# Kernel tuning notes

Hardware: AMD Instinct MI355X
Metric: run time of the kernel (lower is better)

The kernel has to match this reference:

```python
import jax, jax.numpy as jnp
import numpy as np

DIM = 1536
N_HEADS = 12
HEAD_DIM = DIM // N_HEADS  # 128
EPS = 1e-6
B, L = 2, 2048


def _rms_norm(x, g, eps=EPS):
    # WanRMSNorm: normalize in fp32 over last dim, scale by g
    xf = x.astype(jnp.float32)
    y = xf * jax.lax.rsqrt(jnp.mean(xf * xf, axis=-1, keepdims=True) + eps)
    return (y * g).astype(x.dtype)


def _apply_rotary(x, freqs):
    # x: [b, s, n, d]; freqs: [1, s, 2d] -> cos/sin each [1, s, 1, d]
    cos, sin = jnp.split(freqs[:, :, None, :], 2, axis=-1)
    b, s, n, d = x.shape
    xr = x.reshape(b, s, n, d // 2, 2)
    rot = jnp.stack([-xr[..., 1], xr[..., 0]], axis=-1).reshape(b, s, n, d)
    out = x.astype(jnp.float32) * cos + rot.astype(jnp.float32) * sin
    return out.astype(x.dtype)


def setup_inputs() -> dict:
    key = jax.random.key(0)
    ks = jax.random.split(key, 12)
    scale = 1.0 / np.sqrt(DIM)
    x = jax.random.normal(ks[0], (B, L, DIM), dtype=jnp.float32)
    wq = jax.random.normal(ks[1], (DIM, DIM), dtype=jnp.float32) * scale
    bq = jnp.zeros((DIM,), dtype=jnp.float32)
    wk = jax.random.normal(ks[2], (DIM, DIM), dtype=jnp.float32) * scale
    bk = jnp.zeros((DIM,), dtype=jnp.float32)
    wv = jax.random.normal(ks[3], (DIM, DIM), dtype=jnp.float32) * scale
    bv = jnp.zeros((DIM,), dtype=jnp.float32)
    wo = jax.random.normal(ks[4], (DIM, DIM), dtype=jnp.float32) * scale
    bo = jnp.zeros((DIM,), dtype=jnp.float32)
    gq = jnp.ones((DIM,), dtype=jnp.float32)
    gk = jnp.ones((DIM,), dtype=jnp.float32)
    # real RoPE table: interleaved-pair cos/sin, concatenated -> [1, L, 2*HEAD_DIM]
    half = HEAD_DIM // 2
    inv_freq = 1.0 / (10000.0 ** (np.arange(half, dtype=np.float32) / half))
    ang = np.arange(L, dtype=np.float32)[:, None] * inv_freq[None, :]  # [L, half]
    cos = np.repeat(np.cos(ang), 2, axis=-1)  # [L, HEAD_DIM]
    sin = np.repeat(np.sin(ang), 2, axis=-1)
    freqs = jnp.asarray(np.concatenate([cos, sin], axis=-1)[None])  # [1, L, 2*HEAD_DIM]
    seq_lens = jnp.array([L, 3 * L // 4], dtype=jnp.int32)
    grid_sizes = jnp.array([[16, 16, 8], [16, 12, 8]], dtype=jnp.int32)
    return {"x": x, "wq": wq, "bq": bq, "wk": wk, "bk": bk, "wv": wv, "bv": bv,
            "wo": wo, "bo": bo, "gq": gq, "gk": gk, "freqs": freqs,
            "seq_lens": seq_lens, "grid_sizes": grid_sizes}


def reference(x, wq, bq, wk, bk, wv, bv, wo, bo, gq, gk, freqs, seq_lens, grid_sizes):
    b, s, _ = x.shape
    n, d = N_HEADS, HEAD_DIM
    q = _rms_norm(x @ wq.T + bq, gq).reshape(b, s, n, d)
    k = _rms_norm(x @ wk.T + bk, gk).reshape(b, s, n, d)
    v = (x @ wv.T + bv).reshape(b, s, n, d)
    q = _apply_rotary(q, freqs)
    k = _apply_rotary(k, freqs)
    # variable-length attention: mask keys j >= seq_lens[b]; window (-1,-1) = full
    scores = jnp.einsum("bqnd,bknd->bnqk", q, k) * (1.0 / np.sqrt(d))
    key_mask = (jnp.arange(s)[None, :] < seq_lens[:, None])[:, None, None, :]  # [b,1,1,s]
    scores = jnp.where(key_mask, scores, jnp.finfo(scores.dtype).min)
    probs = jax.nn.softmax(scores, axis=-1)
    out = jnp.einsum("bnqk,bknd->bqnd", probs, v).reshape(b, s, n * d)
    return out @ wo.T + bo
```

## Files before the change

kernel.cpp:

```cpp
#include <hip/hip_runtime.h>
#include <stdint.h>

typedef unsigned short u16;
typedef __bf16 bfx8 __attribute__((ext_vector_type(8)));
typedef short  sx4  __attribute__((ext_vector_type(4)));
typedef float  fx4  __attribute__((ext_vector_type(4)));
typedef float  fx16 __attribute__((ext_vector_type(16)));
typedef u16    ux8  __attribute__((ext_vector_type(8)));
typedef u16    ux4  __attribute__((ext_vector_type(4)));
typedef float  flt4 __attribute__((ext_vector_type(4)));

#define DIM   1536
#define NH    12
#define HD    128
#define BATCH 2
#define SEQ   2048
#define MTOK  (BATCH*SEQ)
#define EPSV  1e-6f
#define SCALE 0.08838834764831845f
#define NX    (MTOK*DIM)
#define NW    (DIM*DIM)

__device__ __forceinline__ u16 f2bf(float x){
  union { float f; uint32_t u; } v; v.f = x;
  return (u16)((v.u + 0x7FFFu + ((v.u >> 16) & 1u)) >> 16);
}
__device__ __forceinline__ float bf2f(u16 h){
  union { uint32_t u; float f; } v; v.u = ((uint32_t)h) << 16; return v.f;
}
__device__ __forceinline__ void gl_lds16(const void* g, void* l){
  __builtin_amdgcn_global_load_lds((const __attribute__((address_space(1))) void*)g,
                                   (__attribute__((address_space(3))) void*)l, 16, 0, 0);
}
__device__ __forceinline__ fx4 fzero(){ fx4 z = {0.f,0.f,0.f,0.f}; return z; }

__global__ __launch_bounds__(256)
void convert_k(const float* __restrict__ x, const float* __restrict__ wq,
               const float* __restrict__ wk, const float* __restrict__ wv,
               const float* __restrict__ wo,
               u16* __restrict__ xb, u16* __restrict__ wqb, u16* __restrict__ wkb,
               u16* __restrict__ wvb, u16* __restrict__ wob)
{
  const long i4 = (long)(blockIdx.x * 256 + threadIdx.x) * 4;
  const float* src; u16* dst; long off;
  if (i4 < NX){ src = x; dst = xb; off = i4; }
  else {
    long j = i4 - NX;
    if      (j < (long)NW)   { src = wq; dst = wqb; off = j; }
    else if (j < 2L*NW)      { src = wk; dst = wkb; off = j - NW; }
    else if (j < 3L*NW)      { src = wv; dst = wvb; off = j - 2L*NW; }
    else                     { src = wo; dst = wob; off = j - 3L*NW; }
  }
  flt4 v = *(const flt4*)(src + off);
  ux4 o;
  o[0] = f2bf(v[0]); o[1] = f2bf(v[1]); o[2] = f2bf(v[2]); o[3] = f2bf(v[3]);
  *(ux4*)(dst + off) = o;
}

#define BM 128
#define BN 128
#define BK 64

template<int MODE>
__device__ __forceinline__ void gemm_core(u16* sA, u16* sB,
                                          const u16* __restrict__ A, const u16* __restrict__ W,
                                          const float* __restrict__ bias,
                                          u16* __restrict__ outb, float* __restrict__ outf,
                                          float* __restrict__ sumsq)
{
  const int t = threadIdx.x;
  const int lane = t & 63;
  const int wid = t >> 6;
  const int wm = wid >> 1, wn = wid & 1;
  const int quad = lane >> 4, l15 = lane & 15;
  const int m0 = blockIdx.y * BM;
  const int n0 = blockIdx.x * BN;

  fx4 acc[4][4];
  #pragma unroll
  for (int i = 0; i < 4; ++i)
    #pragma unroll
    for (int j = 0; j < 4; ++j) acc[i][j] = fzero();

  const int ri  = t >> 3;
  const int sg0 = t & 7;

  for (int kb = 0; kb < DIM/BK; ++kb){
    const int k0 = kb * BK;
    #pragma unroll
    for (int s = 0; s < 4; ++s){
      const int row = s*32 + ri;
      const int sa = sg0 ^ (row & 7);
      gl_lds16(A + (m0+row)*DIM + k0 + sa*8, (char*)sA + s*4096 + t*16);
      gl_lds16(W + (n0+row)*DIM + k0 + sa*8, (char*)sB + s*4096 + t*16);
    }
    __syncthreads();
    #pragma unroll
    for (int kk = 0; kk < 2; ++kk){
      bfx8 af[4], bw[4];
      #pragma unroll
      for (int i = 0; i < 4; ++i){
        const int rA = wm*64 + i*16 + l15;
        af[i] = *(const bfx8*)((const char*)sA + rA*128 + (((kk*4 + quad) ^ (rA & 7)) * 16));
        const int rB = wn*64 + i*16 + l15;
        bw[i] = *(const bfx8*)((const char*)sB + rB*128 + (((kk*4 + quad) ^ (rB & 7)) * 16));
      }
      #pragma unroll
      for (int i = 0; i < 4; ++i)
        #pragma unroll
        for (int j = 0; j < 4; ++j)
          acc[i][j] = __builtin_amdgcn_mfma_f32_16x16x32_bf16(af[i], bw[j], acc[i][j], 0, 0, 0);
    }
    __syncthreads();
  }

  float bvals[4];
  #pragma unroll
  for (int j = 0; j < 4; ++j) bvals[j] = bias[n0 + wn*64 + j*16 + l15];

  #pragma unroll
  for (int i = 0; i < 4; ++i){
    #pragma unroll
    for (int r = 0; r < 4; ++r){
      const int grow = m0 + wm*64 + i*16 + quad*4 + r;
      float s2 = 0.f;
      #pragma unroll
      for (int j = 0; j < 4; ++j){
        const int gcol = n0 + wn*64 + j*16 + l15;
        const float v = acc[i][j][r] + bvals[j];
        if (MODE == 2) outf[grow*DIM + gcol] = v;
        else           outb[grow*DIM + gcol] = f2bf(v);
        s2 += v*v;
      }
      if (MODE == 0){
        s2 += __shfl_xor(s2, 1);
        s2 += __shfl_xor(s2, 2);
        s2 += __shfl_xor(s2, 4);
        s2 += __shfl_xor(s2, 8);
        if (l15 == 0) atomicAdd(&sumsq[grow], s2);
      }
    }
  }
}

__global__ __launch_bounds__(256)
void gemm_qkv_k(const u16* __restrict__ xb,
                const u16* __restrict__ wqb, const u16* __restrict__ wkb, const u16* __restrict__ wvb,
                const float* __restrict__ bq, const float* __restrict__ bk, const float* __restrict__ bv,
                u16* __restrict__ qraw, u16* __restrict__ kraw, u16* __restrict__ vraw,
                float* __restrict__ ssq, float* __restrict__ ssk)
{
  __shared__ u16 sA[BM*BK];
  __shared__ u16 sB[BN*BK];
  const int z = blockIdx.z;
  if (z == 0)      gemm_core<0>(sA, sB, xb, wqb, bq, qraw, nullptr, ssq);
  else if (z == 1) gemm_core<0>(sA, sB, xb, wkb, bk, kraw, nullptr, ssk);
  else             gemm_core<1>(sA, sB, xb, wvb, bv, vraw, nullptr, nullptr);
}

__global__ __launch_bounds__(256)
void gemm_out_k(const u16* __restrict__ attnb, const u16* __restrict__ wob,
                const float* __restrict__ bo, float* __restrict__ out)
{
  __shared__ u16 sA[BM*BK];
  __shared__ u16 sB[BN*BK];
  gemm_core<2>(sA, sB, attnb, wob, bo, nullptr, out, nullptr);
}

__global__ __launch_bounds__(256)
void normrope_k(const u16* __restrict__ qraw, const u16* __restrict__ kraw,
                const float* __restrict__ ssq, const float* __restrict__ ssk,
                const float* __restrict__ gq, const float* __restrict__ gk,
                const float* __restrict__ freqs,
                u16* __restrict__ qbf, u16* __restrict__ kbf)
{
  const int row = blockIdx.x;
  const int isK = blockIdx.y;
  const u16* src   = isK ? kraw : qraw;
  const float* ss  = isK ? ssk  : ssq;
  const float* g   = isK ? gk   : gq;
  u16* dst         = isK ? kbf  : qbf;
  const int spos = row & (SEQ - 1);
  float rstd = rsqrtf(ss[row] * (1.0f/DIM) + EPSV);
  if (!isK) rstd *= SCALE;
  #pragma unroll
  for (int it = 0; it < 3; ++it){
    const int p = threadIdx.x + it*256;
    const int d = p*2;
    const int hd = d & (HD-1);
    const uint32_t two = *(const uint32_t*)(src + row*DIM + d);
    const float y0 = bf2f((u16)(two & 0xFFFFu)) * rstd * g[d];
    const float y1 = bf2f((u16)(two >> 16))     * rstd * g[d+1];
    const float c  = freqs[spos*(2*HD) + hd];
    const float sn = freqs[spos*(2*HD) + HD + hd];
    const float o0 = y0*c - y1*sn;
    const float o1 = y1*c + y0*sn;
    *(uint32_t*)(dst + row*DIM + d) = (uint32_t)f2bf(o0) | ((uint32_t)f2bf(o1) << 16);
  }
}

__global__ __launch_bounds__(256)
void transpose_v_k(const u16* __restrict__ v, u16* __restrict__ vt)
{
  __shared__ u16 tile[64][65];
  const int t  = threadIdx.x;
  const int b  = blockIdx.z;
  const int t0 = blockIdx.x * 64;
  const int g0 = blockIdx.y * 64;
  const int r8 = t >> 3;
  const int c8 = (t & 7) * 8;
  #pragma unroll
  for (int i = 0; i < 2; ++i){
    const int row = i*32 + r8;
    ux8 val = *(const ux8*)(v + (b*SEQ + t0 + row)*DIM + g0 + c8);
    #pragma unroll
    for (int j = 0; j < 8; ++j) tile[c8 + j][row] = val[j];
  }
  __syncthreads();
  #pragma unroll
  for (int i = 0; i < 2; ++i){
    const int drow = i*32 + r8;
    const int dg = g0 + drow;
    const int h = dg >> 7, dd = dg & (HD-1);
    ux8 o;
    #pragma unroll
    for (int j = 0; j < 8; ++j) o[j] = tile[drow][c8 + j];
    *(ux8*)(vt + ((b*NH + h)*HD + dd)*SEQ + t0 + c8) = o;
  }
}

__global__ __launch_bounds__(256, 3)
void flash_k(const u16* __restrict__ qbf, const u16* __restrict__ kbf, const u16* __restrict__ vt,
             const int* __restrict__ seq_lens, u16* __restrict__ attnb)
{
  __shared__ char smem[49152];
  const int t = threadIdx.x;
  const int lane = t & 63;
  const int h = lane >> 5;
  const int l31 = lane & 31;
  const int wq = (t >> 6) & 1;
  const int wk = t >> 7;
  const int hh = blockIdx.y, b = blockIdx.z;
  const int q0 = blockIdx.x * 64 + wq * 32;
  const int tokbase = b * SEQ;
  const int kvlen = min(seq_lens[b], SEQ);
  const int ntiles = (kvlen + 63) >> 6;

  bfx8 qf[8];
  {
    const u16* qp = qbf + (size_t)(tokbase + q0 + l31)*DIM + hh*HD + h*8;
    #pragma unroll
    for (int c = 0; c < 8; ++c) qf[c] = *(const bfx8*)(qp + c*16);
  }

  fx16 o[4];
  #pragma unroll
  for (int dt = 0; dt < 4; ++dt)
    #pragma unroll
    for (int r = 0; r < 16; ++r) o[dt][r] = 0.f;
  float mrow = -1e30f, lrow = 0.f;

  const int kri = t >> 4, kseg = t & 15;
  const int vri = t >> 3, vseg = t & 7;
  const int krow = wk*32 + l31;

  for (int kt = 0; kt < ntiles; ++kt){
    {
      #pragma unroll
      for (int s = 0; s < 4; ++s){
        const int row = s*16 + kri;
        const int sg = kseg ^ (row & 15);
        gl_lds16(kbf + (size_t)(tokbase + kt*64 + row)*DIM + hh*HD + sg*8, smem + s*4096 + t*16);
      }
    }
    {
      #pragma unroll
      for (int s = 0; s < 4; ++s){
        const int row = s*32 + vri;
        const int sg = vseg ^ (row & 7);
        gl_lds16(vt + (size_t)((b*NH + hh)*HD + row)*SEQ + kt*64 + sg*8, smem + 16384 + s*4096 + t*16);
      }
    }
    __syncthreads();

    fx16 st;
    #pragma unroll
    for (int r = 0; r < 16; ++r) st[r] = 0.f;
    #pragma unroll
    for (int c = 0; c < 8; ++c){
      const bfx8 kf = *(const bfx8*)(smem + krow*256 + (((2*c + h) ^ (krow & 15)) << 4));
      st = __builtin_amdgcn_mfma_f32_32x32x16_bf16(kf, qf[c], st, 0, 0, 0);
    }

    if ((kt == ntiles - 1) && (kvlen & 63)){
      #pragma unroll
      for (int r = 0; r < 16; ++r){
        const int key = kt*64 + wk*32 + (r & 3) + 8*(r >> 2) + 4*h;
        if (key >= kvlen) st[r] = -1e30f;
      }
    }

    float tm = st[0];
    #pragma unroll
    for (int r = 1; r < 16; ++r) tm = fmaxf(tm, st[r]);
    tm = fmaxf(tm, __shfl_xor(tm, 32));
    if (__any(tm > mrow)){
      const float mnew = fmaxf(mrow, tm);
      const float alpha = __expf(mrow - mnew);
      lrow *= alpha;
      #pragma unroll
      for (int dt = 0; dt < 4; ++dt)
        #pragma unroll
        for (int r = 0; r < 16; ++r) o[dt][r] *= alpha;
      mrow = mnew;
    }

    uint32_t tt[16];
    float ps = 0.f;
    #pragma unroll
    for (int r = 0; r < 16; ++r){
      union { float f; uint32_t u; } e; e.f = __expf(st[r] - mrow);
      const uint32_t u = e.u + 0x8000u;
      tt[r] = u;
      union { uint32_t u; float f; } pm; pm.u = u & 0xFFFF0000u;
      ps += pm.f;
    }
    ps += __shfl_xor(ps, 32);
    lrow += ps;

    sx4 pb[4];
    #pragma unroll
    for (int ks = 0; ks < 4; ++ks){
      union { uint32_t u[2]; sx4 s; } pk;
      pk.u[0] = __builtin_amdgcn_perm(tt[4*ks+1], tt[4*ks+0], 0x07060302u);
      pk.u[1] = __builtin_amdgcn_perm(tt[4*ks+3], tt[4*ks+2], 0x07060302u);
      pb[ks] = pk.s;
    }

    #pragma unroll
    for (int ks = 0; ks < 4; ++ks){
      #pragma unroll
      for (int dt = 0; dt < 4; ++dt){
        const int row = dt*32 + l31;
        const sx4 vf = *(const sx4*)(smem + 16384 + row*128 + ((((wk<<2) + ks) ^ (row & 7)) << 4) + (h << 3));
        o[dt] = __builtin_amdgcn_mfma_f32_32x32x8bf16_1k(vf, pb[ks], o[dt], 0, 0, 0);
      }
    }
    __syncthreads();
  }

  float* mlbuf = (float*)(smem + 32768);
  if (h == 0){
    mlbuf[((wk*2 + wq)*2 + 0)*32 + l31] = mrow;
    mlbuf[((wk*2 + wq)*2 + 1)*32 + l31] = lrow;
  }
  __syncthreads();
  const float mo = mlbuf[(((wk^1)*2 + wq)*2 + 0)*32 + l31];
  const float lo = mlbuf[(((wk^1)*2 + wq)*2 + 1)*32 + l31];
  const float M  = fmaxf(mrow, mo);
  const float f  = __expf(mrow - M);
  const float L  = lrow * f + lo * __expf(mo - M);
  #pragma unroll
  for (int dt = 0; dt < 4; ++dt)
    #pragma unroll
    for (int r = 0; r < 16; ++r) o[dt][r] *= f;
  __syncthreads();

  float* xbuf = (float*)smem;
  if (wk == 1){
    #pragma unroll
    for (int dt = 0; dt < 4; ++dt)
      #pragma unroll
      for (int rq = 0; rq < 4; ++rq){
        const int d = dt*32 + 8*rq + 4*h;
        fx4 v4; v4[0]=o[dt][4*rq]; v4[1]=o[dt][4*rq+1]; v4[2]=o[dt][4*rq+2]; v4[3]=o[dt][4*rq+3];
        *(fx4*)(xbuf + (size_t)(wq*32 + l31)*128 + d) = v4;
      }
  }
  __syncthreads();

  u16* Os = (u16*)(smem + 32768);
  if (wk == 0){
    const float invL = 1.0f / L;
    #pragma unroll
    for (int dt = 0; dt < 4; ++dt)
      #pragma unroll
      for (int rq = 0; rq < 4; ++rq){
        const int d = dt*32 + 8*rq + 4*h;
        const fx4 p4 = *(const fx4*)(xbuf + (size_t)(wq*32 + l31)*128 + d);
        ux4 b4;
        #pragma unroll
        for (int j = 0; j < 4; ++j) b4[j] = f2bf((o[dt][4*rq + j] + p4[j]) * invL);
        *(ux4*)(Os + (size_t)(wq*32 + l31)*128 + d) = b4;
      }
  }
  __syncthreads();
  {
    const int ri = t >> 4, seg = t & 15;
    #pragma unroll
    for (int s = 0; s < 4; ++s){
      const int row = s*16 + ri;
      const ux8 val = *(const ux8*)(Os + row*128 + seg*8);
      *(ux8*)(attnb + (size_t)(tokbase + blockIdx.x*64 + row)*DIM + hh*HD + seg*8) = val;
    }
  }
}

extern "C" void kernel_launch(void* const* d_in, const int* in_sizes, int n_in,
                              void* d_out, int out_size, void* d_ws, size_t ws_size,
                              hipStream_t stream)
{
  (void)in_sizes; (void)n_in; (void)out_size; (void)ws_size;
  const float* x      = (const float*)d_in[0];
  const float* wq     = (const float*)d_in[1];
  const float* bq     = (const float*)d_in[2];
  const float* wk     = (const float*)d_in[3];
  const float* bk     = (const float*)d_in[4];
  const float* wv     = (const float*)d_in[5];
  const float* bv     = (const float*)d_in[6];
  const float* wo     = (const float*)d_in[7];
  const float* bo     = (const float*)d_in[8];
  const float* gq     = (const float*)d_in[9];
  const float* gk     = (const float*)d_in[10];
  const float* freqs  = (const float*)d_in[11];
  const int*   seqls  = (const int*)d_in[12];

  char* ws = (char*)d_ws;
  u16* xb   = (u16*)(ws + 0);
  u16* wqb  = (u16*)(ws + 12582912);
  u16* wkb  = (u16*)(ws + 17301504);
  u16* wvb  = (u16*)(ws + 22020096);
  u16* wob  = (u16*)(ws + 26738688);
  u16* qraw = (u16*)(ws + 31457280);
  u16* kraw = (u16*)(ws + 44040192);
  u16* vraw = (u16*)(ws + 56623104);
  u16* qbf  = (u16*)(ws + 69206016);
  u16* kbf  = (u16*)(ws + 81788928);
  float* ssq = (float*)(ws + 94371840);
  float* ssk = (float*)(ws + 94388224);
  u16* vt    = xb;
  u16* attnb = qraw;

  (void)hipMemsetAsync(ssq, 0, 32768, stream);

  convert_k   <<<15360, 256, 0, stream>>>(x, wq, wk, wv, wo, xb, wqb, wkb, wvb, wob);
  gemm_qkv_k  <<<dim3(12, 32, 3), 256, 0, stream>>>(xb, wqb, wkb, wvb, bq, bk, bv,
                                                    qraw, kraw, vraw, ssq, ssk);
  normrope_k  <<<dim3(4096, 2), 256, 0, stream>>>(qraw, kraw, ssq, ssk, gq, gk, freqs, qbf, kbf);
  transpose_v_k<<<dim3(32, 24, 2), 256, 0, stream>>>(vraw, vt);
  flash_k     <<<dim3(32, 12, 2), 256, 0, stream>>>(qbf, kbf, vt, seqls, attnb);
  gemm_out_k  <<<dim3(12, 32), 256, 0, stream>>>(attnb, wob, bo, (float*)d_out);
}
```

Baseline: 344.6 us.

## Double-buffer GEMM LDS, fuse V transpose into QKV GEMM, remap block order

The GEMM main loop now double-buffers its LDS tiles, issuing loads for the next K block before computing the current one, so there is one barrier per iteration instead of two. The V projection writes its result transposed through an LDS staging tile straight into the per-head layout, which removes the separate transpose kernel and one round trip of V through global memory. GEMM and flash-attention block indices are remapped so that neighbouring workgroups share rows and heads, aiming at better L2 locality. The cost is doubling LDS to 64KB per block, which may lower occupancy.

```diff
diff --git a/kernel.cpp b/kernel.cpp
--- a/kernel.cpp
+++ b/kernel.cpp
@@ -60,21 +60,25 @@
 #define BM 128
 #define BN 128
 #define BK 64
+#define NKIT (DIM/BK)
 
 template<int MODE>
-__device__ __forceinline__ void gemm_core(u16* sA, u16* sB,
+__device__ __forceinline__ void gemm_core(char* smem,
                                           const u16* __restrict__ A, const u16* __restrict__ W,
                                           const float* __restrict__ bias,
                                           u16* __restrict__ outb, float* __restrict__ outf,
-                                          float* __restrict__ sumsq)
+                                          float* __restrict__ sumsq, u16* __restrict__ vtout)
 {
   const int t = threadIdx.x;
   const int lane = t & 63;
   const int wid = t >> 6;
   const int wm = wid >> 1, wn = wid & 1;
   const int quad = lane >> 4, l15 = lane & 15;
-  const int m0 = blockIdx.y * BM;
-  const int n0 = blockIdx.x * BN;
+
+  const int lin = blockIdx.y * 12 + blockIdx.x;
+  const int r   = lin >> 3;
+  const int m0  = ((lin & 7) + 8 * (r / 12)) * BM;
+  const int n0  = (r % 12) * BN;
 
   fx4 acc[4][4];
   #pragma unroll
@@ -85,25 +89,32 @@
   const int ri  = t >> 3;
   const int sg0 = t & 7;
 
-  for (int kb = 0; kb < DIM/BK; ++kb){
+  auto stage = [&](int kb, int p){
     const int k0 = kb * BK;
+    char* base = smem + p * 32768;
     #pragma unroll
     for (int s = 0; s < 4; ++s){
       const int row = s*32 + ri;
       const int sa = sg0 ^ (row & 7);
-      gl_lds16(A + (m0+row)*DIM + k0 + sa*8, (char*)sA + s*4096 + t*16);
-      gl_lds16(W + (n0+row)*DIM + k0 + sa*8, (char*)sB + s*4096 + t*16);
-    }
+      gl_lds16(A + (size_t)(m0+row)*DIM + k0 + sa*8, base + s*4096 + t*16);
+      gl_lds16(W + (size_t)(n0+row)*DIM + k0 + sa*8, base + 16384 + s*4096 + t*16);
+    }
+  };
+
+  stage(0, 0);
+  for (int kb = 0; kb < NKIT; ++kb){
+    char* cur = smem + (kb & 1) * 32768;
     __syncthreads();
+    if (kb + 1 < NKIT) stage(kb + 1, (kb + 1) & 1);
     #pragma unroll
     for (int kk = 0; kk < 2; ++kk){
       bfx8 af[4], bw[4];
       #pragma unroll
       for (int i = 0; i < 4; ++i){
         const int rA = wm*64 + i*16 + l15;
-        af[i] = *(const bfx8*)((const char*)sA + rA*128 + (((kk*4 + quad) ^ (rA & 7)) * 16));
+        af[i] = *(const bfx8*)(cur + rA*128 + (((kk*4 + quad) ^ (rA & 7)) * 16));
         const int rB = wn*64 + i*16 + l15;
-        bw[i] = *(const bfx8*)((const char*)sB + rB*128 + (((kk*4 + quad) ^ (rB & 7)) * 16));
+        bw[i] = *(const bfx8*)(cur + 16384 + rB*128 + (((kk*4 + quad) ^ (rB & 7)) * 16));
       }
       #pragma unroll
       for (int i = 0; i < 4; ++i)
@@ -111,25 +122,55 @@
         for (int j = 0; j < 4; ++j)
           acc[i][j] = __builtin_amdgcn_mfma_f32_16x16x32_bf16(af[i], bw[j], acc[i][j], 0, 0, 0);
     }
+  }
+
+  float bvals[4];
+  #pragma unroll
+  for (int j = 0; j < 4; ++j) bvals[j] = bias[n0 + wn*64 + j*16 + l15];
+
+  if (MODE == 1){
+    u16* T = (u16*)smem;
+    #pragma unroll
+    for (int i = 0; i < 4; ++i){
+      const int row0  = wm*64 + i*16 + quad*4;
+      const int chunk = row0 >> 3;
+      const int half  = quad & 1;
+      #pragma unroll
+      for (int j = 0; j < 4; ++j){
+        const int col = wn*64 + j*16 + l15;
+        ux4 w4;
+        #pragma unroll
+        for (int rr = 0; rr < 4; ++rr) w4[rr] = f2bf(acc[i][j][rr] + bvals[j]);
+        *(ux4*)((char*)T + col*256 + ((chunk ^ (col & 15)) << 4) + half*8) = w4;
+      }
+    }
     __syncthreads();
-  }
-
-  float bvals[4];
-  #pragma unroll
-  for (int j = 0; j < 4; ++j) bvals[j] = bias[n0 + wn*64 + j*16 + l15];
+    const int b   = m0 >> 11;
+    const int m0l = m0 & (SEQ - 1);
+    const int cr  = t & 15;
+    #pragma unroll
+    for (int s = 0; s < 8; ++s){
+      const int cl = s*16 + (t >> 4);
+      const ux8 v = *(const ux8*)((char*)T + cl*256 + ((cr ^ (cl & 15)) << 4));
+      const int cg = n0 + cl;
+      const int hh = cg >> 7, dd = cg & (HD - 1);
+      *(ux8*)(vtout + (size_t)((b*NH + hh)*HD + dd)*SEQ + m0l + cr*8) = v;
+    }
+    return;
+  }
 
   #pragma unroll
   for (int i = 0; i < 4; ++i){
     #pragma unroll
-    for (int r = 0; r < 4; ++r){
-      const int grow = m0 + wm*64 + i*16 + quad*4 + r;
+    for (int rr = 0; rr < 4; ++rr){
+      const int grow = m0 + wm*64 + i*16 + quad*4 + rr;
       float s2 = 0.f;
       #pragma unroll
       for (int j = 0; j < 4; ++j){
         const int gcol = n0 + wn*64 + j*16 + l15;
-        const float v = acc[i][j][r] + bvals[j];
-        if (MODE == 2) outf[grow*DIM + gcol] = v;
-        else           outb[grow*DIM + gcol] = f2bf(v);
+        const float v = acc[i][j][rr] + bvals[j];
+        if (MODE == 2) outf[(size_t)grow*DIM + gcol] = v;
+        else           outb[(size_t)grow*DIM + gcol] = f2bf(v);
         s2 += v*v;
       }
       if (MODE == 0){
@@ -147,24 +188,22 @@
 void gemm_qkv_k(const u16* __restrict__ xb,
                 const u16* __restrict__ wqb, const u16* __restrict__ wkb, const u16* __restrict__ wvb,
                 const float* __restrict__ bq, const float* __restrict__ bk, const float* __restrict__ bv,
-                u16* __restrict__ qraw, u16* __restrict__ kraw, u16* __restrict__ vraw,
+                u16* __restrict__ qraw, u16* __restrict__ kraw, u16* __restrict__ vt,
                 float* __restrict__ ssq, float* __restrict__ ssk)
 {
-  __shared__ u16 sA[BM*BK];
-  __shared__ u16 sB[BN*BK];
+  __shared__ char smem[65536];
   const int z = blockIdx.z;
-  if (z == 0)      gemm_core<0>(sA, sB, xb, wqb, bq, qraw, nullptr, ssq);
-  else if (z == 1) gemm_core<0>(sA, sB, xb, wkb, bk, kraw, nullptr, ssk);
-  else             gemm_core<1>(sA, sB, xb, wvb, bv, vraw, nullptr, nullptr);
+  if (z == 0)      gemm_core<0>(smem, xb, wqb, bq, qraw, nullptr, ssq, nullptr);
+  else if (z == 1) gemm_core<0>(smem, xb, wkb, bk, kraw, nullptr, ssk, nullptr);
+  else             gemm_core<1>(smem, xb, wvb, bv, nullptr, nullptr, nullptr, vt);
 }
 
 __global__ __launch_bounds__(256)
 void gemm_out_k(const u16* __restrict__ attnb, const u16* __restrict__ wob,
                 const float* __restrict__ bo, float* __restrict__ out)
 {
-  __shared__ u16 sA[BM*BK];
-  __shared__ u16 sB[BN*BK];
-  gemm_core<2>(sA, sB, attnb, wob, bo, nullptr, out, nullptr);
+  __shared__ char smem[65536];
+  gemm_core<2>(smem, attnb, wob, bo, nullptr, out, nullptr, nullptr);
 }
 
 __global__ __launch_bounds__(256)
@@ -188,44 +227,14 @@
     const int p = threadIdx.x + it*256;
     const int d = p*2;
     const int hd = d & (HD-1);
-    const uint32_t two = *(const uint32_t*)(src + row*DIM + d);
+    const uint32_t two = *(const uint32_t*)(src + (size_t)row*DIM + d);
     const float y0 = bf2f((u16)(two & 0xFFFFu)) * rstd * g[d];
     const float y1 = bf2f((u16)(two >> 16))     * rstd * g[d+1];
     const float c  = freqs[spos*(2*HD) + hd];
     const float sn = freqs[spos*(2*HD) + HD + hd];
     const float o0 = y0*c - y1*sn;
     const float o1 = y1*c + y0*sn;
-    *(uint32_t*)(dst + row*DIM + d) = (uint32_t)f2bf(o0) | ((uint32_t)f2bf(o1) << 16);
-  }
-}
-
-__global__ __launch_bounds__(256)
-void transpose_v_k(const u16* __restrict__ v, u16* __restrict__ vt)
-{
-  __shared__ u16 tile[64][65];
-  const int t  = threadIdx.x;
-  const int b  = blockIdx.z;
-  const int t0 = blockIdx.x * 64;
-  const int g0 = blockIdx.y * 64;
-  const int r8 = t >> 3;
-  const int c8 = (t & 7) * 8;
-  #pragma unroll
-  for (int i = 0; i < 2; ++i){
-    const int row = i*32 + r8;
-    ux8 val = *(const ux8*)(v + (b*SEQ + t0 + row)*DIM + g0 + c8);
-    #pragma unroll
-    for (int j = 0; j < 8; ++j) tile[c8 + j][row] = val[j];
-  }
-  __syncthreads();
-  #pragma unroll
-  for (int i = 0; i < 2; ++i){
-    const int drow = i*32 + r8;
-    const int dg = g0 + drow;
-    const int h = dg >> 7, dd = dg & (HD-1);
-    ux8 o;
-    #pragma unroll
-    for (int j = 0; j < 8; ++j) o[j] = tile[drow][c8 + j];
-    *(ux8*)(vt + ((b*NH + h)*HD + dd)*SEQ + t0 + c8) = o;
+    *(uint32_t*)(dst + (size_t)row*DIM + d) = (uint32_t)f2bf(o0) | ((uint32_t)f2bf(o1) << 16);
   }
 }
 
@@ -240,8 +249,14 @@
   const int l31 = lane & 31;
   const int wq = (t >> 6) & 1;
   const int wk = t >> 7;
-  const int hh = blockIdx.y, b = blockIdx.z;
-  const int q0 = blockIdx.x * 64 + wq * 32;
+
+  const int u  = blockIdx.x;
+  const int qt = (u >> 3) & 31;
+  const int pr = (u & 7) + 8 * (u >> 8);
+  const int hh = pr % 12;
+  const int b  = pr / 12;
+
+  const int q0 = qt * 64 + wq * 32;
   const int tokbase = b * SEQ;
   const int kvlen = min(seq_lens[b], SEQ);
   const int ntiles = (kvlen + 63) >> 6;
@@ -320,9 +335,9 @@
     #pragma unroll
     for (int r = 0; r < 16; ++r){
       union { float f; uint32_t u; } e; e.f = __expf(st[r] - mrow);
-      const uint32_t u = e.u + 0x8000u;
-      tt[r] = u;
-      union { uint32_t u; float f; } pm; pm.u = u & 0xFFFF0000u;
+      const uint32_t uu = e.u + 0x8000u;
+      tt[r] = uu;
+      union { uint32_t u; float f; } pm; pm.u = uu & 0xFFFF0000u;
       ps += pm.f;
     }
     ps += __shfl_xor(ps, 32);
@@ -401,7 +416,7 @@
     for (int s = 0; s < 4; ++s){
       const int row = s*16 + ri;
       const ux8 val = *(const ux8*)(Os + row*128 + seg*8);
-      *(ux8*)(attnb + (size_t)(tokbase + blockIdx.x*64 + row)*DIM + hh*HD + seg*8) = val;
+      *(ux8*)(attnb + (size_t)(tokbase + qt*64 + row)*DIM + hh*HD + seg*8) = val;
     }
   }
 }
@@ -433,21 +448,19 @@
   u16* wob  = (u16*)(ws + 26738688);
   u16* qraw = (u16*)(ws + 31457280);
   u16* kraw = (u16*)(ws + 44040192);
-  u16* vraw = (u16*)(ws + 56623104);
+  u16* vt   = (u16*)(ws + 56623104);
   u16* qbf  = (u16*)(ws + 69206016);
   u16* kbf  = (u16*)(ws + 81788928);
   float* ssq = (float*)(ws + 94371840);
   float* ssk = (float*)(ws + 94388224);
-  u16* vt    = xb;
   u16* attnb = qraw;
 
   (void)hipMemsetAsync(ssq, 0, 32768, stream);
 
   convert_k   <<<15360, 256, 0, stream>>>(x, wq, wk, wv, wo, xb, wqb, wkb, wvb, wob);
   gemm_qkv_k  <<<dim3(12, 32, 3), 256, 0, stream>>>(xb, wqb, wkb, wvb, bq, bk, bv,
-                                                    qraw, kraw, vraw, ssq, ssk);
+                                                    qraw, kraw, vt, ssq, ssk);
   normrope_k  <<<dim3(4096, 2), 256, 0, stream>>>(qraw, kraw, ssq, ssk, gq, gk, freqs, qbf, kbf);
-  transpose_v_k<<<dim3(32, 24, 2), 256, 0, stream>>>(vraw, vt);
-  flash_k     <<<dim3(32, 12, 2), 256, 0, stream>>>(qbf, kbf, vt, seqls, attnb);
+  flash_k     <<<dim3(768), 256, 0, stream>>>(qbf, kbf, vt, seqls, attnb);
   gemm_out_k  <<<dim3(12, 32), 256, 0, stream>>>(attnb, wob, bo, (float*)d_out);
 }
```

After: 316.3 us. 1.09x faster.
